# Optimization experiments

Hardware: AMD Instinct MI355X
Metric: run time of the kernel (lower is better)

The kernel has to match this reference:

```python
import jax, jax.numpy as jnp
import numpy as np

N, E, D = 50000, 600000, 128
NUM_BOND_TYPE, NUM_BOND_DIR = 5, 3
SELF_LOOP_TYPE = 4  # self-loop edge_attr = [4, 0]


def setup_inputs() -> dict:
    key = jax.random.key(0)
    ks = jax.random.split(key, 10)
    x = jax.random.normal(ks[0], (N, D), dtype=jnp.float32)
    edge_index = jax.random.randint(ks[1], (2, E), 0, N, dtype=jnp.int64)
    edge_attr = jax.random.randint(ks[2], (E, 2), 0, 3, dtype=jnp.int64)
    # learned params (torch Linear: y = x @ W.T + b)
    s1 = 1.0 / np.sqrt(D)
    s2 = 1.0 / np.sqrt(2 * D)
    W1 = jax.random.uniform(ks[3], (2 * D, D), jnp.float32, -s1, s1)
    b1 = jax.random.uniform(ks[4], (2 * D,), jnp.float32, -s1, s1)
    W2 = jax.random.uniform(ks[5], (D, 2 * D), jnp.float32, -s2, s2)
    b2 = jax.random.uniform(ks[6], (D,), jnp.float32, -s2, s2)
    e1 = jax.random.normal(ks[7], (NUM_BOND_TYPE, D), jnp.float32) * np.sqrt(2.0 / (NUM_BOND_TYPE + D))
    e2 = jax.random.normal(ks[8], (NUM_BOND_DIR, D), jnp.float32) * np.sqrt(2.0 / (NUM_BOND_DIR + D))
    return {"x": x, "edge_index": edge_index, "edge_attr": edge_attr,
            "W1": W1, "b1": b1, "W2": W2, "b2": b2, "e1": e1, "e2": e2}


def reference(x, edge_index, edge_attr, W1, b1, W2, b2, e1, e2):
    row, col = edge_index[0], edge_index[1]
    # edge embeddings for the real edges: [E, D]
    edge_emb = e1[edge_attr[:, 0]] + e2[edge_attr[:, 1]]
    # messages gathered from source nodes, scatter-added to destinations
    messages = x[col] + edge_emb  # [E, D]
    out = jax.ops.segment_sum(messages, row, num_segments=N)
    # self-loops: add_self_loops appends edge (i,i) with attr [4,0] for each node,
    # contributing x[i] + e1[4] + e2[0] to out[i]; add it directly (same math).
    out = out + x + e1[SELF_LOOP_TYPE] + e2[0]
    # 2-layer MLP
    h = jax.nn.relu(out @ W1.T + b1)
    return h @ W2.T + b2
```

## Files before the change

kernel.cpp:

```cpp
#include <hip/hip_runtime.h>

#define N_NODES 50000
#define N_EDGES 600000
#define DIM 128

#define CAP 64
#define GRID_E 2344
#define BLK_ROWS 32

#define WS_CNT_OFF   0
#define WS_PERM_OFF  200000
#define WS_XB_OFF    13000000
#define WS_W1B_OFF   25800000
#define WS_W2B_OFF   25865536

#define CVT_X4   1600000
#define CVT_W4   8192
#define CVT_TOTAL (CVT_X4 + 2*CVT_W4)
#define CVT_BLOCKS ((CVT_TOTAL + 255) / 256)
#define ZERO_BLOCKS 196

typedef __attribute__((ext_vector_type(8))) short bf16x8;
typedef __attribute__((ext_vector_type(4))) float f32x4;

__device__ __forceinline__ unsigned short f2bf(float f) {
    unsigned int b = __float_as_uint(f);
    b += 0x7FFFu + ((b >> 16) & 1u);
    return (unsigned short)(b >> 16);
}
__device__ __forceinline__ float bf2f(short u) {
    return __uint_as_float(((unsigned int)(unsigned short)u) << 16);
}

__global__ __launch_bounds__(256) void place_kernel(
    const int* __restrict__ eidx, const int* __restrict__ eattr,
    int* __restrict__ cnt, unsigned int* __restrict__ perm)
{
    int e = blockIdx.x * 256 + threadIdx.x;
    if (e >= N_EDGES) return;
    int row = eidx[e];
    unsigned int col = (unsigned int)eidx[N_EDGES + e];
    unsigned int a0  = (unsigned int)eattr[2 * e];
    unsigned int a1  = (unsigned int)eattr[2 * e + 1];
    int pos = atomicAdd(&cnt[row], 1);
    if (pos < CAP)
        perm[(size_t)row * CAP + pos] = col | (a0 << 16) | (a1 << 19);
}

__global__ __launch_bounds__(256) void cvt_all_kernel(
    const float* __restrict__ x, const float* __restrict__ W1,
    const float* __restrict__ W2, unsigned short* __restrict__ xb,
    unsigned short* __restrict__ w1b, unsigned short* __restrict__ w2b,
    int* __restrict__ cnt)
{
    if (blockIdx.x >= CVT_BLOCKS) {
        int j = (blockIdx.x - CVT_BLOCKS) * 256 + threadIdx.x;
        if (j < N_NODES) cnt[j] = 0;
        return;
    }
    int i = blockIdx.x * 256 + threadIdx.x;
    if (i < CVT_X4) {
        float4 v = reinterpret_cast<const float4*>(x)[i];
        reinterpret_cast<ushort4*>(xb)[i] =
            make_ushort4(f2bf(v.x), f2bf(v.y), f2bf(v.z), f2bf(v.w));
    } else if (i < CVT_X4 + CVT_W4) {
        int j = i - CVT_X4;
        float4 v = reinterpret_cast<const float4*>(W1)[j];
        reinterpret_cast<ushort4*>(w1b)[j] =
            make_ushort4(f2bf(v.x), f2bf(v.y), f2bf(v.z), f2bf(v.w));
    } else if (i < CVT_TOTAL) {
        int j = i - CVT_X4 - CVT_W4;
        float4 v = reinterpret_cast<const float4*>(W2)[j];
        reinterpret_cast<ushort4*>(w2b)[j] =
            make_ushort4(f2bf(v.x), f2bf(v.y), f2bf(v.z), f2bf(v.w));
    }
}

__global__ __launch_bounds__(256) void fused_mlp_kernel(
    const float* __restrict__ x, const unsigned short* __restrict__ xb,
    const float* __restrict__ e1, const float* __restrict__ e2,
    const unsigned int* __restrict__ perm, const int* __restrict__ cnt,
    const unsigned short* __restrict__ w1b, const float* __restrict__ b1,
    const unsigned short* __restrict__ w2b, const float* __restrict__ b2,
    float* __restrict__ Y)
{
    __shared__ __align__(16) unsigned short sA[BLK_ROWS][136];
    __shared__ __align__(16) unsigned short sH[2][16][264];

    int t = threadIdx.x;

    {
        int ln = t & 15;
        int c0 = ln * 8;
        #pragma unroll
        for (int pass = 0; pass < 2; ++pass) {
            int n = (t >> 4) + pass * 16;
            int g = blockIdx.x * BLK_ROWS + n;
            float acc[8];
            if (g < N_NODES) {
                const float* xr = x + (size_t)g * DIM + c0;
                float4 s0 = *reinterpret_cast<const float4*>(xr);
                float4 s1 = *reinterpret_cast<const float4*>(xr + 4);
                acc[0] = s0.x; acc[1] = s0.y; acc[2] = s0.z; acc[3] = s0.w;
                acc[4] = s1.x; acc[5] = s1.y; acc[6] = s1.z; acc[7] = s1.w;

                unsigned long long cnt0 = 1ull << (12 * 4);
                unsigned int       cnt1 = 1u;

                int ne = cnt[g]; if (ne > CAP) ne = CAP;
                const unsigned int* pp = perm + (size_t)g * CAP;
                int e = 0;
                for (; e + 4 <= ne; e += 4) {
                    uint4 uu = *reinterpret_cast<const uint4*>(pp + e);
                    bf16x8 x0 = *reinterpret_cast<const bf16x8*>(xb + (size_t)(uu.x & 0xFFFFu) * DIM + c0);
                    bf16x8 x1 = *reinterpret_cast<const bf16x8*>(xb + (size_t)(uu.y & 0xFFFFu) * DIM + c0);
                    bf16x8 x2 = *reinterpret_cast<const bf16x8*>(xb + (size_t)(uu.z & 0xFFFFu) * DIM + c0);
                    bf16x8 x3 = *reinterpret_cast<const bf16x8*>(xb + (size_t)(uu.w & 0xFFFFu) * DIM + c0);
                    cnt0 += (1ull << (12 * ((uu.x >> 16) & 7u)))
                          + (1ull << (12 * ((uu.y >> 16) & 7u)))
                          + (1ull << (12 * ((uu.z >> 16) & 7u)))
                          + (1ull << (12 * ((uu.w >> 16) & 7u)));
                    cnt1 += (1u << (10 * (uu.x >> 19))) + (1u << (10 * (uu.y >> 19)))
                          + (1u << (10 * (uu.z >> 19))) + (1u << (10 * (uu.w >> 19)));
                    #pragma unroll
                    for (int j = 0; j < 8; ++j)
                        acc[j] += (bf2f(x0[j]) + bf2f(x1[j])) + (bf2f(x2[j]) + bf2f(x3[j]));
                }
                for (; e < ne; ++e) {
                    unsigned int u = pp[e];
                    bf16x8 xv = *reinterpret_cast<const bf16x8*>(xb + (size_t)(u & 0xFFFFu) * DIM + c0);
                    cnt0 += 1ull << (12 * ((u >> 16) & 7u));
                    cnt1 += 1u << (10 * (u >> 19));
                    #pragma unroll
                    for (int j = 0; j < 8; ++j) acc[j] += bf2f(xv[j]);
                }

                #pragma unroll
                for (int tt = 0; tt < 5; ++tt) {
                    float m = (float)((unsigned int)((cnt0 >> (12 * tt)) & 0xFFFu));
                    const float* er = e1 + tt * DIM + c0;
                    float4 u0 = *reinterpret_cast<const float4*>(er);
                    float4 u1 = *reinterpret_cast<const float4*>(er + 4);
                    acc[0] += m * u0.x; acc[1] += m * u0.y;
                    acc[2] += m * u0.z; acc[3] += m * u0.w;
                    acc[4] += m * u1.x; acc[5] += m * u1.y;
                    acc[6] += m * u1.z; acc[7] += m * u1.w;
                }
                #pragma unroll
                for (int tt = 0; tt < 3; ++tt) {
                    float m = (float)((cnt1 >> (10 * tt)) & 0x3FFu);
                    const float* er = e2 + tt * DIM + c0;
                    float4 u0 = *reinterpret_cast<const float4*>(er);
                    float4 u1 = *reinterpret_cast<const float4*>(er + 4);
                    acc[0] += m * u0.x; acc[1] += m * u0.y;
                    acc[2] += m * u0.z; acc[3] += m * u0.w;
                    acc[4] += m * u1.x; acc[5] += m * u1.y;
                    acc[6] += m * u1.z; acc[7] += m * u1.w;
                }
            } else {
                #pragma unroll
                for (int j = 0; j < 8; ++j) acc[j] = 0.f;
            }
            bf16x8 o;
            #pragma unroll
            for (int j = 0; j < 8; ++j) o[j] = (short)f2bf(acc[j]);
            *reinterpret_cast<bf16x8*>(&sA[n][c0]) = o;
        }
    }
    __syncthreads();

    int wid  = t >> 6;
    int pair = wid >> 1;
    int sub  = wid & 1;
    int l    = t & 63;
    int l16  = l & 15;
    int lhi  = l >> 4;
    int rowbase = blockIdx.x * BLK_ROWS + pair * 16;

    bf16x8 af[4];
    #pragma unroll
    for (int kk = 0; kk < 4; ++kk)
        af[kk] = *reinterpret_cast<const bf16x8*>(&sA[pair * 16 + l16][kk * 32 + lhi * 8]);

    float tb1[8];
    #pragma unroll
    for (int i = 0; i < 8; ++i) tb1[i] = b1[(sub * 8 + i) * 16 + l16];

    f32x4 acc1[8];
    #pragma unroll
    for (int i = 0; i < 8; ++i) acc1[i] = (f32x4){0.f, 0.f, 0.f, 0.f};

    #pragma unroll
    for (int kk = 0; kk < 4; ++kk) {
        bf16x8 wf[8];
        #pragma unroll
        for (int i = 0; i < 8; ++i)
            wf[i] = *reinterpret_cast<const bf16x8*>(
                w1b + (size_t)((sub * 8 + i) * 16 + l16) * DIM + kk * 32 + lhi * 8);
        #pragma unroll
        for (int i = 0; i < 8; ++i)
            acc1[i] = __builtin_amdgcn_mfma_f32_16x16x32_bf16(af[kk], wf[i], acc1[i], 0, 0, 0);
    }
    #pragma unroll
    for (int i = 0; i < 8; ++i) {
        int n0 = (sub * 8 + i) * 16;
        #pragma unroll
        for (int r = 0; r < 4; ++r)
            sH[pair][lhi * 4 + r][n0 + l16] = f2bf(fmaxf(acc1[i][r] + tb1[i], 0.f));
    }
    __syncthreads();

    float tb2[4];
    #pragma unroll
    for (int i = 0; i < 4; ++i) tb2[i] = b2[(sub * 4 + i) * 16 + l16];

    f32x4 acc2[4];
    #pragma unroll
    for (int i = 0; i < 4; ++i) acc2[i] = (f32x4){0.f, 0.f, 0.f, 0.f};

    #pragma unroll
    for (int kk = 0; kk < 8; ++kk) {
        bf16x8 hf = *reinterpret_cast<const bf16x8*>(&sH[pair][l16][kk * 32 + lhi * 8]);
        bf16x8 wf[4];
        #pragma unroll
        for (int i = 0; i < 4; ++i)
            wf[i] = *reinterpret_cast<const bf16x8*>(
                w2b + (size_t)((sub * 4 + i) * 16 + l16) * 256 + kk * 32 + lhi * 8);
        #pragma unroll
        for (int i = 0; i < 4; ++i)
            acc2[i] = __builtin_amdgcn_mfma_f32_16x16x32_bf16(hf, wf[i], acc2[i], 0, 0, 0);
    }
    #pragma unroll
    for (int i = 0; i < 4; ++i) {
        int n0 = (sub * 4 + i) * 16;
        #pragma unroll
        for (int r = 0; r < 4; ++r) {
            int grow = rowbase + lhi * 4 + r;
            if (grow < N_NODES)
                Y[(size_t)grow * DIM + n0 + l16] = acc2[i][r] + tb2[i];
        }
    }
}

extern "C" void kernel_launch(void* const* d_in, const int* in_sizes, int n_in,
                              void* d_out, int out_size, void* d_ws, size_t ws_size,
                              hipStream_t stream)
{
    const float* x   = (const float*)d_in[0];
    const int*  eidx = (const int*)d_in[1];
    const int*  eattr= (const int*)d_in[2];
    const float* W1  = (const float*)d_in[3];
    const float* b1  = (const float*)d_in[4];
    const float* W2  = (const float*)d_in[5];
    const float* b2  = (const float*)d_in[6];
    const float* e1  = (const float*)d_in[7];
    const float* e2  = (const float*)d_in[8];
    float* Y = (float*)d_out;

    char* ws = (char*)d_ws;
    int* cnt             = (int*)(ws + WS_CNT_OFF);
    unsigned int* perm   = (unsigned int*)(ws + WS_PERM_OFF);
    unsigned short* xb   = (unsigned short*)(ws + WS_XB_OFF);
    unsigned short* w1b  = (unsigned short*)(ws + WS_W1B_OFF);
    unsigned short* w2b  = (unsigned short*)(ws + WS_W2B_OFF);

    cvt_all_kernel  <<<CVT_BLOCKS + ZERO_BLOCKS, 256, 0, stream>>>(
                        x, W1, W2, xb, w1b, w2b, cnt);
    place_kernel    <<<GRID_E, 256, 0, stream>>>(eidx, eattr, cnt, perm);
    fused_mlp_kernel<<<(N_NODES + BLK_ROWS - 1) / BLK_ROWS, 256, 0, stream>>>(
                        x, xb, e1, e2, perm, cnt, w1b, b1, w2b, b2, Y);
}
```

Before: 137.5 us.

## Halve fused block rows and gather eight neighbors per iteration with padded dummy row

Blocks in the fused aggregate+MLP kernel now cover 16 rows instead of 32, so each thread aggregates one node rather than looping two passes, and the four waves split the MLP output columns rather than pairing up over rows. The gather loop issues eight neighbor loads per iteration, filling the tail with a dummy index that points at a zeroed padding row appended to the bf16 copy of x and at unused type slots in the packed counters. This drops the scalar tail loop and raises memory-level parallelism and grid size. In exchange, each block reloads the W1/W2 fragments for only half as many rows, and perm reads may run past the valid entries into the CAP-sized slot.

New measurement: 118.7 us. -13.7%, faster.

```diff
diff --git a/kernel.cpp b/kernel.cpp
--- a/kernel.cpp
+++ b/kernel.cpp
@@ -6,17 +6,21 @@
 
 #define CAP 64
 #define GRID_E 2344
-#define BLK_ROWS 32
+#define BLK_ROWS 16
+#define GRID_FUSED 3125
+
+#define DUMMY (50000u | (5u << 16) | (3u << 19))
 
 #define WS_CNT_OFF   0
 #define WS_PERM_OFF  200000
 #define WS_XB_OFF    13000000
-#define WS_W1B_OFF   25800000
-#define WS_W2B_OFF   25865536
-
-#define CVT_X4   1600000
-#define CVT_W4   8192
-#define CVT_TOTAL (CVT_X4 + 2*CVT_W4)
+#define WS_W1B_OFF   25800256
+#define WS_W2B_OFF   25865792
+
+#define CVT_X4    1600000
+#define CVT_XROWS 1600032
+#define CVT_W4    8192
+#define CVT_TOTAL (CVT_XROWS + 2 * CVT_W4)
 #define CVT_BLOCKS ((CVT_TOTAL + 255) / 256)
 #define ZERO_BLOCKS 196
 
@@ -63,13 +67,15 @@
         float4 v = reinterpret_cast<const float4*>(x)[i];
         reinterpret_cast<ushort4*>(xb)[i] =
             make_ushort4(f2bf(v.x), f2bf(v.y), f2bf(v.z), f2bf(v.w));
-    } else if (i < CVT_X4 + CVT_W4) {
-        int j = i - CVT_X4;
+    } else if (i < CVT_XROWS) {
+        reinterpret_cast<ushort4*>(xb)[i] = make_ushort4(0, 0, 0, 0);
+    } else if (i < CVT_XROWS + CVT_W4) {
+        int j = i - CVT_XROWS;
         float4 v = reinterpret_cast<const float4*>(W1)[j];
         reinterpret_cast<ushort4*>(w1b)[j] =
             make_ushort4(f2bf(v.x), f2bf(v.y), f2bf(v.z), f2bf(v.w));
     } else if (i < CVT_TOTAL) {
-        int j = i - CVT_X4 - CVT_W4;
+        int j = i - CVT_XROWS - CVT_W4;
         float4 v = reinterpret_cast<const float4*>(W2)[j];
         reinterpret_cast<ushort4*>(w2b)[j] =
             make_ushort4(f2bf(v.x), f2bf(v.y), f2bf(v.z), f2bf(v.w));
@@ -84,161 +90,151 @@
     const unsigned short* __restrict__ w2b, const float* __restrict__ b2,
     float* __restrict__ Y)
 {
-    __shared__ __align__(16) unsigned short sA[BLK_ROWS][136];
-    __shared__ __align__(16) unsigned short sH[2][16][264];
+    __shared__ __align__(16) unsigned short sA[16][136];
+    __shared__ __align__(16) unsigned short sH[16][264];
 
     int t = threadIdx.x;
 
     {
-        int ln = t & 15;
-        int c0 = ln * 8;
-        #pragma unroll
-        for (int pass = 0; pass < 2; ++pass) {
-            int n = (t >> 4) + pass * 16;
-            int g = blockIdx.x * BLK_ROWS + n;
-            float acc[8];
-            if (g < N_NODES) {
-                const float* xr = x + (size_t)g * DIM + c0;
-                float4 s0 = *reinterpret_cast<const float4*>(xr);
-                float4 s1 = *reinterpret_cast<const float4*>(xr + 4);
-                acc[0] = s0.x; acc[1] = s0.y; acc[2] = s0.z; acc[3] = s0.w;
-                acc[4] = s1.x; acc[5] = s1.y; acc[6] = s1.z; acc[7] = s1.w;
-
-                unsigned long long cnt0 = 1ull << (12 * 4);
-                unsigned int       cnt1 = 1u;
-
-                int ne = cnt[g]; if (ne > CAP) ne = CAP;
-                const unsigned int* pp = perm + (size_t)g * CAP;
-                int e = 0;
-                for (; e + 4 <= ne; e += 4) {
-                    uint4 uu = *reinterpret_cast<const uint4*>(pp + e);
-                    bf16x8 x0 = *reinterpret_cast<const bf16x8*>(xb + (size_t)(uu.x & 0xFFFFu) * DIM + c0);
-                    bf16x8 x1 = *reinterpret_cast<const bf16x8*>(xb + (size_t)(uu.y & 0xFFFFu) * DIM + c0);
-                    bf16x8 x2 = *reinterpret_cast<const bf16x8*>(xb + (size_t)(uu.z & 0xFFFFu) * DIM + c0);
-                    bf16x8 x3 = *reinterpret_cast<const bf16x8*>(xb + (size_t)(uu.w & 0xFFFFu) * DIM + c0);
-                    cnt0 += (1ull << (12 * ((uu.x >> 16) & 7u)))
-                          + (1ull << (12 * ((uu.y >> 16) & 7u)))
-                          + (1ull << (12 * ((uu.z >> 16) & 7u)))
-                          + (1ull << (12 * ((uu.w >> 16) & 7u)));
-                    cnt1 += (1u << (10 * (uu.x >> 19))) + (1u << (10 * (uu.y >> 19)))
-                          + (1u << (10 * (uu.z >> 19))) + (1u << (10 * (uu.w >> 19)));
-                    #pragma unroll
-                    for (int j = 0; j < 8; ++j)
-                        acc[j] += (bf2f(x0[j]) + bf2f(x1[j])) + (bf2f(x2[j]) + bf2f(x3[j]));
-                }
-                for (; e < ne; ++e) {
-                    unsigned int u = pp[e];
-                    bf16x8 xv = *reinterpret_cast<const bf16x8*>(xb + (size_t)(u & 0xFFFFu) * DIM + c0);
-                    cnt0 += 1ull << (12 * ((u >> 16) & 7u));
-                    cnt1 += 1u << (10 * (u >> 19));
-                    #pragma unroll
-                    for (int j = 0; j < 8; ++j) acc[j] += bf2f(xv[j]);
-                }
-
-                #pragma unroll
-                for (int tt = 0; tt < 5; ++tt) {
-                    float m = (float)((unsigned int)((cnt0 >> (12 * tt)) & 0xFFFu));
-                    const float* er = e1 + tt * DIM + c0;
-                    float4 u0 = *reinterpret_cast<const float4*>(er);
-                    float4 u1 = *reinterpret_cast<const float4*>(er + 4);
-                    acc[0] += m * u0.x; acc[1] += m * u0.y;
-                    acc[2] += m * u0.z; acc[3] += m * u0.w;
-                    acc[4] += m * u1.x; acc[5] += m * u1.y;
-                    acc[6] += m * u1.z; acc[7] += m * u1.w;
-                }
-                #pragma unroll
-                for (int tt = 0; tt < 3; ++tt) {
-                    float m = (float)((cnt1 >> (10 * tt)) & 0x3FFu);
-                    const float* er = e2 + tt * DIM + c0;
-                    float4 u0 = *reinterpret_cast<const float4*>(er);
-                    float4 u1 = *reinterpret_cast<const float4*>(er + 4);
-                    acc[0] += m * u0.x; acc[1] += m * u0.y;
-                    acc[2] += m * u0.z; acc[3] += m * u0.w;
-                    acc[4] += m * u1.x; acc[5] += m * u1.y;
-                    acc[6] += m * u1.z; acc[7] += m * u1.w;
-                }
-            } else {
-                #pragma unroll
-                for (int j = 0; j < 8; ++j) acc[j] = 0.f;
+        int n  = t >> 4;
+        int g  = blockIdx.x * BLK_ROWS + n;
+        int ln = t & 15, c0 = ln * 8;
+
+        const float* xr = x + (size_t)g * DIM + c0;
+        float4 s0 = *reinterpret_cast<const float4*>(xr);
+        float4 s1 = *reinterpret_cast<const float4*>(xr + 4);
+
+        int ne = cnt[g]; if (ne > CAP) ne = CAP;
+        const uint4* pp4 = reinterpret_cast<const uint4*>(perm + (size_t)g * CAP);
+
+        unsigned long long c0v = 1ull << 48;
+        unsigned int       c1v = 1u;
+        float acc[8] = {0.f, 0.f, 0.f, 0.f, 0.f, 0.f, 0.f, 0.f};
+
+        for (int e = 0; e < ne; e += 8) {
+            int i0 = e >> 2;
+            uint4 a = pp4[i0];
+            uint4 b = pp4[i0 + 1];
+            unsigned ua[8] = {a.x, a.y, a.z, a.w, b.x, b.y, b.z, b.w};
+            #pragma unroll
+            for (int q = 0; q < 8; ++q)
+                if (e + q >= ne) ua[q] = DUMMY;
+            bf16x8 xv[8];
+            #pragma unroll
+            for (int q = 0; q < 8; ++q)
+                xv[q] = *reinterpret_cast<const bf16x8*>(
+                    xb + (size_t)(ua[q] & 0xFFFFu) * DIM + c0);
+            #pragma unroll
+            for (int q = 0; q < 8; ++q) {
+                c0v += 1ull << (12 * ((ua[q] >> 16) & 7u));
+                c1v += 1u   << (10 * (ua[q] >> 19));
             }
-            bf16x8 o;
-            #pragma unroll
-            for (int j = 0; j < 8; ++j) o[j] = (short)f2bf(acc[j]);
-            *reinterpret_cast<bf16x8*>(&sA[n][c0]) = o;
+            #pragma unroll
+            for (int j = 0; j < 8; ++j)
+                acc[j] += ((bf2f(xv[0][j]) + bf2f(xv[1][j])) +
+                           (bf2f(xv[2][j]) + bf2f(xv[3][j]))) +
+                          ((bf2f(xv[4][j]) + bf2f(xv[5][j])) +
+                           (bf2f(xv[6][j]) + bf2f(xv[7][j])));
         }
+
+        acc[0] += s0.x; acc[1] += s0.y; acc[2] += s0.z; acc[3] += s0.w;
+        acc[4] += s1.x; acc[5] += s1.y; acc[6] += s1.z; acc[7] += s1.w;
+
+        #pragma unroll
+        for (int tt = 0; tt < 5; ++tt) {
+            float m = (float)((unsigned int)((c0v >> (12 * tt)) & 0xFFFu));
+            const float* er = e1 + tt * DIM + c0;
+            float4 u0 = *reinterpret_cast<const float4*>(er);
+            float4 u1 = *reinterpret_cast<const float4*>(er + 4);
+            acc[0] += m * u0.x; acc[1] += m * u0.y;
+            acc[2] += m * u0.z; acc[3] += m * u0.w;
+            acc[4] += m * u1.x; acc[5] += m * u1.y;
+            acc[6] += m * u1.z; acc[7] += m * u1.w;
+        }
+        #pragma unroll
+        for (int tt = 0; tt < 3; ++tt) {
+            float m = (float)((c1v >> (10 * tt)) & 0x3FFu);
+            const float* er = e2 + tt * DIM + c0;
+            float4 u0 = *reinterpret_cast<const float4*>(er);
+            float4 u1 = *reinterpret_cast<const float4*>(er + 4);
+            acc[0] += m * u0.x; acc[1] += m * u0.y;
+            acc[2] += m * u0.z; acc[3] += m * u0.w;
+            acc[4] += m * u1.x; acc[5] += m * u1.y;
+            acc[6] += m * u1.z; acc[7] += m * u1.w;
+        }
+
+        bf16x8 o;
+        #pragma unroll
+        for (int j = 0; j < 8; ++j) o[j] = (short)f2bf(acc[j]);
+        *reinterpret_cast<bf16x8*>(&sA[n][c0]) = o;
     }
     __syncthreads();
 
-    int wid  = t >> 6;
-    int pair = wid >> 1;
-    int sub  = wid & 1;
-    int l    = t & 63;
-    int l16  = l & 15;
-    int lhi  = l >> 4;
-    int rowbase = blockIdx.x * BLK_ROWS + pair * 16;
+    int wid = t >> 6;
+    int l   = t & 63;
+    int l16 = l & 15;
+    int lhi = l >> 4;
+    int rowbase = blockIdx.x * BLK_ROWS;
 
     bf16x8 af[4];
     #pragma unroll
     for (int kk = 0; kk < 4; ++kk)
-        af[kk] = *reinterpret_cast<const bf16x8*>(&sA[pair * 16 + l16][kk * 32 + lhi * 8]);
-
-    float tb1[8];
-    #pragma unroll
-    for (int i = 0; i < 8; ++i) tb1[i] = b1[(sub * 8 + i) * 16 + l16];
-
-    f32x4 acc1[8];
-    #pragma unroll
-    for (int i = 0; i < 8; ++i) acc1[i] = (f32x4){0.f, 0.f, 0.f, 0.f};
+        af[kk] = *reinterpret_cast<const bf16x8*>(&sA[l16][kk * 32 + lhi * 8]);
+
+    float tb1[4];
+    #pragma unroll
+    for (int i = 0; i < 4; ++i) tb1[i] = b1[(wid * 4 + i) * 16 + l16];
+
+    f32x4 acc1[4];
+    #pragma unroll
+    for (int i = 0; i < 4; ++i) acc1[i] = (f32x4){0.f, 0.f, 0.f, 0.f};
 
     #pragma unroll
     for (int kk = 0; kk < 4; ++kk) {
-        bf16x8 wf[8];
-        #pragma unroll
-        for (int i = 0; i < 8; ++i)
-            wf[i] = *reinterpret_cast<const bf16x8*>(
-                w1b + (size_t)((sub * 8 + i) * 16 + l16) * DIM + kk * 32 + lhi * 8);
-        #pragma unroll
-        for (int i = 0; i < 8; ++i)
-            acc1[i] = __builtin_amdgcn_mfma_f32_16x16x32_bf16(af[kk], wf[i], acc1[i], 0, 0, 0);
-    }
-    #pragma unroll
-    for (int i = 0; i < 8; ++i) {
-        int n0 = (sub * 8 + i) * 16;
-        #pragma unroll
-        for (int r = 0; r < 4; ++r)
-            sH[pair][lhi * 4 + r][n0 + l16] = f2bf(fmaxf(acc1[i][r] + tb1[i], 0.f));
-    }
-    __syncthreads();
-
-    float tb2[4];
-    #pragma unroll
-    for (int i = 0; i < 4; ++i) tb2[i] = b2[(sub * 4 + i) * 16 + l16];
-
-    f32x4 acc2[4];
-    #pragma unroll
-    for (int i = 0; i < 4; ++i) acc2[i] = (f32x4){0.f, 0.f, 0.f, 0.f};
-
-    #pragma unroll
-    for (int kk = 0; kk < 8; ++kk) {
-        bf16x8 hf = *reinterpret_cast<const bf16x8*>(&sH[pair][l16][kk * 32 + lhi * 8]);
         bf16x8 wf[4];
         #pragma unroll
         for (int i = 0; i < 4; ++i)
             wf[i] = *reinterpret_cast<const bf16x8*>(
-                w2b + (size_t)((sub * 4 + i) * 16 + l16) * 256 + kk * 32 + lhi * 8);
+                w1b + (size_t)((wid * 4 + i) * 16 + l16) * DIM + kk * 32 + lhi * 8);
         #pragma unroll
         for (int i = 0; i < 4; ++i)
+            acc1[i] = __builtin_amdgcn_mfma_f32_16x16x32_bf16(af[kk], wf[i], acc1[i], 0, 0, 0);
+    }
+    #pragma unroll
+    for (int i = 0; i < 4; ++i) {
+        int n0 = (wid * 4 + i) * 16;
+        #pragma unroll
+        for (int r = 0; r < 4; ++r)
+            sH[lhi * 4 + r][n0 + l16] = f2bf(fmaxf(acc1[i][r] + tb1[i], 0.f));
+    }
+    __syncthreads();
+
+    float tb2[2];
+    #pragma unroll
+    for (int i = 0; i < 2; ++i) tb2[i] = b2[(wid * 2 + i) * 16 + l16];
+
+    f32x4 acc2[2];
+    #pragma unroll
+    for (int i = 0; i < 2; ++i) acc2[i] = (f32x4){0.f, 0.f, 0.f, 0.f};
+
+    #pragma unroll
+    for (int kk = 0; kk < 8; ++kk) {
+        bf16x8 hf = *reinterpret_cast<const bf16x8*>(&sH[l16][kk * 32 + lhi * 8]);
+        bf16x8 wf[2];
+        #pragma unroll
+        for (int i = 0; i < 2; ++i)
+            wf[i] = *reinterpret_cast<const bf16x8*>(
+                w2b + (size_t)((wid * 2 + i) * 16 + l16) * 256 + kk * 32 + lhi * 8);
+        #pragma unroll
+        for (int i = 0; i < 2; ++i)
             acc2[i] = __builtin_amdgcn_mfma_f32_16x16x32_bf16(hf, wf[i], acc2[i], 0, 0, 0);
     }
     #pragma unroll
-    for (int i = 0; i < 4; ++i) {
-        int n0 = (sub * 4 + i) * 16;
-        #pragma unroll
-        for (int r = 0; r < 4; ++r) {
-            int grow = rowbase + lhi * 4 + r;
-            if (grow < N_NODES)
-                Y[(size_t)grow * DIM + n0 + l16] = acc2[i][r] + tb2[i];
-        }
+    for (int i = 0; i < 2; ++i) {
+        int n0 = (wid * 2 + i) * 16;
+        #pragma unroll
+        for (int r = 0; r < 4; ++r)
+            Y[(size_t)(rowbase + lhi * 4 + r) * DIM + n0 + l16] = acc2[i][r] + tb2[i];
     }
 }
 
@@ -267,6 +263,6 @@
     cvt_all_kernel  <<<CVT_BLOCKS + ZERO_BLOCKS, 256, 0, stream>>>(
                         x, W1, W2, xb, w1b, w2b, cnt);
     place_kernel    <<<GRID_E, 256, 0, stream>>>(eidx, eattr, cnt, perm);
-    fused_mlp_kernel<<<(N_NODES + BLK_ROWS - 1) / BLK_ROWS, 256, 0, stream>>>(
+    fused_mlp_kernel<<<GRID_FUSED, 256, 0, stream>>>(
                         x, xb, e1, e2, perm, cnt, w1b, b1, w2b, b2, Y);
 }
```
